# Kernel tuning notes

Measured on AMD Instinct MI355X. Metric: run time of the kernel, lower is better.

The kernel has to match this reference:

```python
import jax, jax.numpy as jnp
import numpy as np

EPS = 1e-5
HID = 32
FUSED = 33 * 33 * 33  # 35937


def _subnet(x, gamma, beta, W1, b1, W2, b2, W3, b3):
    # BatchNorm1d in training mode: batch mean / biased variance
    mu = jnp.mean(x, axis=0)
    var = jnp.mean((x - mu) ** 2, axis=0)
    xn = (x - mu) / jnp.sqrt(var + EPS) * gamma + beta
    h = jax.nn.relu(xn @ W1 + b1)
    h = jax.nn.relu(h @ W2 + b2)
    return jax.nn.relu(h @ W3 + b3)


def _subnet_params(key, in_dim):
    ks = jax.random.split(key, 6)
    s_in = 1.0 / np.sqrt(in_dim)
    s_h = 1.0 / np.sqrt(HID)
    return dict(
        gamma=jnp.ones((in_dim,), jnp.float32),
        beta=jnp.zeros((in_dim,), jnp.float32),
        W1=jax.random.uniform(ks[0], (in_dim, HID), jnp.float32, -s_in, s_in),
        b1=jax.random.uniform(ks[1], (HID,), jnp.float32, -s_in, s_in),
        W2=jax.random.uniform(ks[2], (HID, HID), jnp.float32, -s_h, s_h),
        b2=jax.random.uniform(ks[3], (HID,), jnp.float32, -s_h, s_h),
        W3=jax.random.uniform(ks[4], (HID, HID), jnp.float32, -s_h, s_h),
        b3=jax.random.uniform(ks[5], (HID,), jnp.float32, -s_h, s_h),
    )


def setup_inputs() -> dict:
    key = jax.random.key(0)
    ks = jax.random.split(key, 10)
    B = 8192
    inp = {
        'US_x': jax.random.normal(ks[0], (B, 1024), jnp.float32),
        'CDFI_x': jax.random.normal(ks[1], (B, 1024), jnp.float32),
        'marker_x': jax.random.normal(ks[2], (B, 10), jnp.float32),
    }
    for pref, k, d in (('us', ks[3], 1024), ('cd', ks[4], 1024), ('mk', ks[5], 10)):
        for n, v in _subnet_params(k, d).items():
            inp[f'{pref}_{n}'] = v
    s1 = 1.0 / np.sqrt(FUSED)
    s2 = 1.0 / np.sqrt(33)
    inp['Wf1'] = jax.random.uniform(ks[6], (FUSED, 33), jnp.float32, -s1, s1)
    inp['bf1'] = jax.random.uniform(ks[7], (33,), jnp.float32, -s1, s1)
    inp['Wf2'] = jax.random.uniform(ks[8], (33, 5), jnp.float32, -s2, s2)
    inp['bf2'] = jax.random.uniform(ks[9], (5,), jnp.float32, -s2, s2)
    return inp


def reference(US_x, CDFI_x, marker_x,
              us_gamma, us_beta, us_W1, us_b1, us_W2, us_b2, us_W3, us_b3,
              cd_gamma, cd_beta, cd_W1, cd_b1, cd_W2, cd_b2, cd_W3, cd_b3,
              mk_gamma, mk_beta, mk_W1, mk_b1, mk_W2, mk_b2, mk_W3, mk_b3,
              Wf1, bf1, Wf2, bf2):
    B = US_x.shape[0]
    us_h = _subnet(US_x, us_gamma, us_beta, us_W1, us_b1, us_W2, us_b2, us_W3, us_b3)
    cd_h = _subnet(CDFI_x, cd_gamma, cd_beta, cd_W1, cd_b1, cd_W2, cd_b2, cd_W3, cd_b3)
    mk_h = _subnet(marker_x, mk_gamma, mk_beta, mk_W1, mk_b1, mk_W2, mk_b2, mk_W3, mk_b3)
    ones = jnp.ones((B, 1), jnp.float32)
    us1 = jnp.concatenate([ones, us_h], axis=1)   # [B,33]
    cd1 = jnp.concatenate([ones, cd_h], axis=1)   # [B,33]
    mk1 = jnp.concatenate([ones, mk_h], axis=1)   # [B,33]
    # fused[b,k,j,i] = mk1[b,k] * cd1[b,j] * us1[b,i]; flattened row-major
    fused = jnp.einsum('bk,bj,bi->bkji', mk1, cd1, us1).reshape(B, FUSED)
    h = jax.nn.relu(fused @ Wf1 + bf1)
    return jax.nn.sigmoid(h @ Wf2 + bf2)
```

## Files before the change

kernel.cpp:

```cpp
#include <hip/hip_runtime.h>
#include <hip/hip_bf16.h>
#include <math.h>

typedef __hip_bfloat16 bf16;
typedef __attribute__((ext_vector_type(4))) float f32x4;
typedef __attribute__((ext_vector_type(8))) short s16x8;

#define NB 8192
#define KP 1152
#define NP 1152
#define NKT 18
#define SBLK 256

struct SubP {
    const float* x; const float* gamma; const float* beta;
    const float* W1; const float* b1; const float* W2; const float* b2;
    const float* W3; const float* b3;
    float* sum; float* sumsq; float* a; float* b1p; float* hout;
    bf16* w1t;
    int F;
};
struct SubP3 { SubP s[3]; };

__global__ void __launch_bounds__(256) stats3_kernel(SubP3 P) {
    const SubP p = P.s[blockIdx.z];
    int t = threadIdx.x;
    int blk = blockIdx.x;
    int row0 = blk * 32;
    if (p.F == 1024) {
        f32x4 s = {0.f, 0.f, 0.f, 0.f}, s2 = {0.f, 0.f, 0.f, 0.f};
        const float* xp = p.x + (size_t)row0 * 1024 + t * 4;
        #pragma unroll 8
        for (int r = 0; r < 32; r++) {
            f32x4 v = *(const f32x4*)(xp + (size_t)r * 1024);
            s += v; s2 += v * v;
        }
        int f = t * 4;
        *(f32x4*)&p.sum[(size_t)blk * 2048 + f]   = s;
        *(f32x4*)&p.sumsq[(size_t)blk * 2048 + f] = s2;
    } else {
        __shared__ float ls[16], ls2[16];
        if (t < 16) { ls[t] = 0.f; ls2[t] = 0.f; }
        __syncthreads();
        int F = p.F;
        for (int idx = t; idx < 32 * F; idx += 256) {
            float v = p.x[(size_t)row0 * F + idx];
            int f = idx % 10;
            atomicAdd(&ls[f], v);
            atomicAdd(&ls2[f], v * v);
        }
        __syncthreads();
        if (t < F) {
            p.sum[(size_t)blk * 2048 + t]   = ls[t];
            p.sumsq[(size_t)blk * 2048 + t] = ls2[t];
        }
    }
}

__global__ void prep3_kernel(SubP3 P) {
    const SubP p = P.s[blockIdx.y];
    int f0 = blockIdx.x * 32;
    if (f0 >= p.F) return;
    int t = threadIdx.x;
    __shared__ float c_sh[32];
    __shared__ float ash[32];
    __shared__ float red[8][33];
    __shared__ float rs[8][33], rs2[8][33];
    int fc = p.F - f0; if (fc > 32) fc = 32;
    int fi = t & 31, g = t >> 5;
    {
        float s = 0.f, s2 = 0.f;
        if (fi < fc) {
            for (int blk = g; blk < SBLK; blk += 8) {
                s  += p.sum[(size_t)blk * 2048 + f0 + fi];
                s2 += p.sumsq[(size_t)blk * 2048 + f0 + fi];
            }
        }
        rs[g][fi] = s; rs2[g][fi] = s2;
    }
    __syncthreads();
    if (t < 32) {
        float c = 0.f, av = 0.f;
        if (t < fc) {
            float sm = 0.f, sq = 0.f;
            #pragma unroll
            for (int gg = 0; gg < 8; gg++) { sm += rs[gg][t]; sq += rs2[gg][t]; }
            int f = f0 + t;
            float mu  = sm * (1.f / 8192.f);
            float var = sq * (1.f / 8192.f) - mu * mu;
            av = p.gamma[f] * rsqrtf(var + 1e-5f);
            p.a[f] = av;
            c = p.beta[f] - mu * av;
        }
        c_sh[t] = c; ash[t] = av;
    }
    __syncthreads();
    int h = t & 31; g = t >> 5;
    float s = 0.f;
    for (int fi2 = g; fi2 < fc; fi2 += 8)
        s += c_sh[fi2] * p.W1[(size_t)(f0 + fi2) * 32 + h];
    red[g][h] = s;
    __syncthreads();
    if (t < 32) {
        float tot = 0.f;
        #pragma unroll
        for (int gg = 0; gg < 8; gg++) tot += red[gg][t];
        atomicAdd(&p.b1p[t], tot);
    }
    if (p.F == 1024) {
        for (int idx = t; idx < 1024; idx += 256) {
            int kk = idx >> 5, hh = idx & 31;
            p.w1t[(size_t)hh * 1024 + f0 + kk] =
                __float2bfloat16(ash[kk] * p.W1[(size_t)(f0 + kk) * 32 + hh]);
        }
    }
}

__global__ void __launch_bounds__(256) subnet3_kernel(SubP3 P) {
    const SubP p = P.s[blockIdx.y];
    const int F = p.F;
    __shared__ float smem[9760];
    float* Red = smem;
    float* H1  = smem + 3456;
    float* W23 = smem + 4608;
    float* H2  = smem;

    int t = threadIdx.x;
    int row0 = blockIdx.x * 32;
    int kg = t >> 6;
    int lane = t & 63;
    int hg = lane & 7, h0 = hg * 4;
    int rg = (lane >> 3) & 3;
    int ks = lane >> 5;

    if (F == 1024) {
        bf16* Xl = (bf16*)(smem + 5664);
        bf16* Wl = (bf16*)(smem + 7712);
        int xr = t >> 3, xc = (t & 7) * 16;
        int sw = xr & 7;
        int s0 = ((t & 7) * 2) ^ sw, s1 = ((t & 7) * 2 + 1) ^ sw;
        const float* xbase = p.x + (size_t)(row0 + xr) * 1024 + xc;
        const bf16*  wbase = p.w1t + (size_t)xr * 1024 + xc;
        f32x4 xp[4]; s16x8 wp0, wp1;
        #pragma unroll
        for (int i = 0; i < 4; i++) xp[i] = *(const f32x4*)(xbase + i * 4);
        wp0 = *(const s16x8*)(wbase);
        wp1 = *(const s16x8*)(wbase + 8);

        f32x4 acc[2][2] = {};
        int fr = lane & 15, qq = lane >> 4;
        int rsw0 = fr & 7;

        for (int c = 0; c < 8; c++) {
            __builtin_amdgcn_s_barrier();
            asm volatile("" ::: "memory");
            {
                s16x8 v0, v1;
                #pragma unroll
                for (int i = 0; i < 2; i++)
                    #pragma unroll
                    for (int e = 0; e < 4; e++) {
                        __hip_bfloat16 hb = __float2bfloat16(xp[i][e]);
                        v0[i * 4 + e] = *(short*)&hb;
                    }
                #pragma unroll
                for (int i = 0; i < 2; i++)
                    #pragma unroll
                    for (int e = 0; e < 4; e++) {
                        __hip_bfloat16 hb = __float2bfloat16(xp[2 + i][e]);
                        v1[i * 4 + e] = *(short*)&hb;
                    }
                *(s16x8*)((char*)Xl + xr * 256 + s0 * 16) = v0;
                *(s16x8*)((char*)Xl + xr * 256 + s1 * 16) = v1;
                *(s16x8*)((char*)Wl + xr * 256 + s0 * 16) = wp0;
                *(s16x8*)((char*)Wl + xr * 256 + s1 * 16) = wp1;
            }
            if (c < 7) {
                int k0 = (c + 1) * 128;
                #pragma unroll
                for (int i = 0; i < 4; i++) xp[i] = *(const f32x4*)(xbase + k0 + i * 4);
                wp0 = *(const s16x8*)(wbase + k0);
                wp1 = *(const s16x8*)(wbase + k0 + 8);
            }
            asm volatile("s_waitcnt lgkmcnt(0)" ::: "memory");
            __builtin_amdgcn_sched_barrier(0);
            __builtin_amdgcn_s_barrier();
            asm volatile("" ::: "memory");
            {
                int sx = kg * 4 + qq;
                int sl = (sx ^ rsw0) * 16;
                s16x8 a0 = *(const s16x8*)((char*)Xl + fr * 256 + sl);
                s16x8 a1 = *(const s16x8*)((char*)Xl + (16 + fr) * 256 + sl);
                s16x8 b0 = *(const s16x8*)((char*)Wl + fr * 256 + sl);
                s16x8 b1 = *(const s16x8*)((char*)Wl + (16 + fr) * 256 + sl);
                acc[0][0] = __builtin_amdgcn_mfma_f32_16x16x32_bf16(a0, b0, acc[0][0], 0, 0, 0);
                acc[0][1] = __builtin_amdgcn_mfma_f32_16x16x32_bf16(a0, b1, acc[0][1], 0, 0, 0);
                acc[1][0] = __builtin_amdgcn_mfma_f32_16x16x32_bf16(a1, b0, acc[1][0], 0, 0, 0);
                acc[1][1] = __builtin_amdgcn_mfma_f32_16x16x32_bf16(a1, b1, acc[1][1], 0, 0, 0);
            }
        }
        int col = lane & 15, rowg = (lane >> 4) * 4;
        if (kg > 0) {
            #pragma unroll
            for (int m = 0; m < 2; m++)
                #pragma unroll
                for (int n = 0; n < 2; n++)
                    #pragma unroll
                    for (int r = 0; r < 4; r++)
                        Red[(kg - 1) * 1152 + (m * 16 + rowg + r) * 36 + n * 16 + col] = acc[m][n][r];
        }
        __syncthreads();
        if (kg == 0) {
            #pragma unroll
            for (int m = 0; m < 2; m++)
                #pragma unroll
                for (int n = 0; n < 2; n++) {
                    int cc = n * 16 + col;
                    float bv = p.b1[cc] + p.b1p[cc];
                    #pragma unroll
                    for (int r = 0; r < 4; r++) {
                        int rr = m * 16 + rowg + r;
                        float v = acc[m][n][r] + bv;
                        #pragma unroll
                        for (int pp = 0; pp < 3; pp++)
                            v += Red[pp * 1152 + rr * 36 + cc];
                        H1[rr * 36 + cc] = fmaxf(v, 0.f);
                    }
                }
        }
    } else {
        float* Xt = smem;
        float* Wt = smem + 2176;
        float acc[4][8] = {};
        int kbase = (kg * 2 + ks) * 8;
        for (int k0 = 0; k0 < F; k0 += 64) {
            int kc = F - k0; if (kc > 64) kc = 64;
            int kcp = (kc + 3) & ~3;
            __syncthreads();
            for (int idx = t; idx < 32 * kcp; idx += 256) {
                int r = idx / kcp, kk = idx - r * kcp;
                Xt[r * 68 + kk] = (kk < kc) ? p.x[(size_t)(row0 + r) * F + k0 + kk] : 0.f;
            }
            for (int idx = t; idx < kcp * 32; idx += 256) {
                int kk = idx >> 5, hh = idx & 31;
                Wt[kk * 36 + hh] = (kk < kc) ? p.a[k0 + kk] * p.W1[(size_t)(k0 + kk) * 32 + hh] : 0.f;
            }
            __syncthreads();
            #pragma unroll
            for (int s = 0; s < 2; s++) {
                int kk = kbase + s * 4;
                if (kk < kcp) {
                    f32x4 wv[4], xv[8];
                    #pragma unroll
                    for (int j = 0; j < 4; j++)  wv[j]  = *(const f32x4*)&Wt[(kk + j) * 36 + h0];
                    #pragma unroll
                    for (int ri = 0; ri < 8; ri++) xv[ri] = *(const f32x4*)&Xt[(rg + 4 * ri) * 68 + kk];
                    #pragma unroll
                    for (int j = 0; j < 4; j++)
                        #pragma unroll
                        for (int hi = 0; hi < 4; hi++) {
                            float w = wv[j][hi];
                            #pragma unroll
                            for (int ri = 0; ri < 8; ri++)
                                acc[hi][ri] = fmaf(w, xv[ri][j], acc[hi][ri]);
                        }
                }
            }
        }
        #pragma unroll
        for (int hi = 0; hi < 4; hi++)
            #pragma unroll
            for (int ri = 0; ri < 8; ri++)
                acc[hi][ri] += __shfl_xor(acc[hi][ri], 32);
        __syncthreads();
        if (kg > 0 && ks == 0) {
            #pragma unroll
            for (int ri = 0; ri < 8; ri++) {
                int r = rg + 4 * ri;
                f32x4 v = {acc[0][ri], acc[1][ri], acc[2][ri], acc[3][ri]};
                *(f32x4*)&Red[(kg - 1) * 1152 + r * 36 + h0] = v;
            }
        }
        __syncthreads();
        if (kg == 0 && ks == 0) {
            f32x4 b;
            #pragma unroll
            for (int hi = 0; hi < 4; hi++) b[hi] = p.b1[h0 + hi] + p.b1p[h0 + hi];
            #pragma unroll
            for (int ri = 0; ri < 8; ri++) {
                int r = rg + 4 * ri;
                f32x4 v = {acc[0][ri], acc[1][ri], acc[2][ri], acc[3][ri]};
                #pragma unroll
                for (int pp = 0; pp < 3; pp++)
                    v += *(const f32x4*)&Red[pp * 1152 + r * 36 + h0];
                v += b;
                #pragma unroll
                for (int hi = 0; hi < 4; hi++)
                    H1[r * 36 + h0 + hi] = fmaxf(v[hi], 0.f);
            }
        }
    }
    for (int idx = t; idx < 1024; idx += 256) W23[(idx >> 5) * 33 + (idx & 31)] = p.W2[idx];
    __syncthreads();
    int h = t & 31, rq = t >> 5;
    {
        float a2[4] = {};
        for (int q = 0; q < 32; q++) {
            float w = W23[q * 33 + h];
            #pragma unroll
            for (int i = 0; i < 4; i++) a2[i] += H1[(rq * 4 + i) * 36 + q] * w;
        }
        float bv = p.b2[h];
        #pragma unroll
        for (int i = 0; i < 4; i++) H2[(rq * 4 + i) * 36 + h] = fmaxf(a2[i] + bv, 0.f);
    }
    __syncthreads();
    for (int idx = t; idx < 1024; idx += 256) W23[(idx >> 5) * 33 + (idx & 31)] = p.W3[idx];
    __syncthreads();
    {
        float a3[4] = {};
        for (int q = 0; q < 32; q++) {
            float w = W23[q * 33 + h];
            #pragma unroll
            for (int i = 0; i < 4; i++) a3[i] += H2[(rq * 4 + i) * 36 + q] * w;
        }
        float bv = p.b3[h];
        #pragma unroll
        for (int i = 0; i < 4; i++)
            p.hout[(size_t)(row0 + rq * 4 + i) * 32 + h] = fmaxf(a3[i] + bv, 0.f);
    }
}

__global__ void __launch_bounds__(256) build_both(const float* __restrict__ mk_h,
                           const float* __restrict__ us_h,
                           bf16* __restrict__ p1,
                           const float* __restrict__ Wf1, bf16* __restrict__ W2t) {
    int blk = blockIdx.x;
    int t = threadIdx.x;
    if (blk < NB / 4) {
        int r = t >> 6, lane = t & 63;
        int b = blk * 4 + r;
        __shared__ float mk1[4][34], us1[4][34];
        if (lane == 0) { mk1[r][0] = 1.f; us1[r][0] = 1.f; }
        if (lane < 32) mk1[r][lane + 1] = mk_h[(size_t)b * 32 + lane];
        else           us1[r][lane - 31] = us_h[(size_t)b * 32 + (lane - 32)];
        __syncthreads();
        #pragma unroll
        for (int c = 0; c < 3; c++) {
            int chunk = lane + 64 * c;
            if (chunk < 144) {
                int base = chunk * 8;
                s16x8 v;
                #pragma unroll
                for (int e = 0; e < 8; e++) {
                    int idx = base + e;
                    float val = 0.f;
                    if (idx < 1089) {
                        int k = idx / 33, i = idx - k * 33;
                        val = mk1[r][k] * us1[r][i];
                    }
                    __hip_bfloat16 hb = __float2bfloat16(val);
                    v[e] = *(short*)&hb;
                }
                *(s16x8*)(p1 + (size_t)b * KP + base) = v;
            }
        }
    } else {
        int kj = blk - NB / 4;
        int k = kj / 33, j = kj - k * 33;
        __shared__ float tile[1089];
        const float* src = Wf1 + (size_t)k * 35937 + (size_t)j * 1089;
        for (int idx = t; idx < 1089; idx += 256) tile[idx] = src[idx];
        __syncthreads();
        for (int idx = t; idx < 1089; idx += 256) {
            int o = idx / 33, i = idx - o * 33;
            W2t[(size_t)(j * 33 + o) * KP + k * 33 + i] = __float2bfloat16(tile[i * 33 + o]);
        }
        if (k == 0) {
            bf16 z = __float2bfloat16(0.f);
            for (int idx = t; idx < 33 * 63; idx += 256) {
                int o = idx / 63, kkp = 1089 + idx - o * 63;
                W2t[(size_t)(j * 33 + o) * KP + kkp] = z;
            }
        }
    }
}

__global__ void __launch_bounds__(512) gemm_kernel(const bf16* __restrict__ A,
                                                   const bf16* __restrict__ Bt,
                                                   bf16* __restrict__ S) {
    __shared__ __align__(16) bf16 As[2][256 * 64];
    __shared__ __align__(16) bf16 Bs[2][192 * 64];
    int t = threadIdx.x;
    int wv = t >> 6, lane = t & 63;
    int m0 = blockIdx.x * 256;
    int n0 = blockIdx.y * 144;
    int fr = lane & 15;
    int q  = lane >> 4;
    int lr8 = lane >> 3;
    int sslot = (lane & 7) ^ lr8;

    const bf16* Ag = A  + (size_t)(m0 + wv * 32 + lr8) * KP + sslot * 8;
    const bf16* Bg = Bt + (size_t)(n0 + wv * 24 + lr8) * KP + sslot * 8;

    f32x4 acc[2][9] = {};

    auto stageA = [&](int buf, int T) {
        bf16* Ad = &As[buf][wv * 32 * 64];
        const bf16* s = Ag + T * 64;
        #pragma unroll
        for (int i = 0; i < 4; i++)
            __builtin_amdgcn_global_load_lds(
                (const __attribute__((address_space(1))) void*)(s + (size_t)i * 8 * KP),
                (__attribute__((address_space(3))) void*)(Ad + i * 512), 16, 0, 0);
    };
    auto stageB = [&](int buf, int T) {
        bf16* Bd = &Bs[buf][wv * 24 * 64];
        const bf16* s = Bg + T * 64;
        #pragma unroll
        for (int c = 0; c < 3; c++)
            __builtin_amdgcn_global_load_lds(
                (const __attribute__((address_space(1))) void*)(s + (size_t)c * 8 * KP),
                (__attribute__((address_space(3))) void*)(Bd + c * 512), 16, 0, 0);
    };

    stageA(0, 0);
    stageB(0, 0);

    for (int T = 0; T < NKT; T++) {
        int b = T & 1;
        const bf16* Ab = &As[b][0];
        const bf16* Bb = &Bs[b][0];
        if (T < NKT - 1) {
            stageA(b ^ 1, T + 1);
            asm volatile("s_waitcnt vmcnt(4)" ::: "memory");
        } else {
            asm volatile("s_waitcnt vmcnt(0)" ::: "memory");
        }
        __builtin_amdgcn_s_barrier();
        asm volatile("" ::: "memory");
        {
            int sl = (q ^ (fr & 7)) * 8;
            s16x8 af0 = *(const s16x8*)(Ab + (wv * 32 + fr) * 64 + sl);
            s16x8 af1 = *(const s16x8*)(Ab + (wv * 32 + 16 + fr) * 64 + sl);
            s16x8 bfv[9];
            #pragma unroll
            for (int n2 = 0; n2 < 9; n2++)
                bfv[n2] = *(const s16x8*)(Bb + (n2 * 16 + fr) * 64 + sl);
            __builtin_amdgcn_s_setprio(1);
            #pragma unroll
            for (int n2 = 0; n2 < 9; n2++) {
                acc[0][n2] = __builtin_amdgcn_mfma_f32_16x16x32_bf16(af0, bfv[n2], acc[0][n2], 0, 0, 0);
                acc[1][n2] = __builtin_amdgcn_mfma_f32_16x16x32_bf16(af1, bfv[n2], acc[1][n2], 0, 0, 0);
            }
            __builtin_amdgcn_s_setprio(0);
        }
        if (T < NKT - 1) stageB(b ^ 1, T + 1);
        {
            int sl = ((4 + q) ^ (fr & 7)) * 8;
            s16x8 af0 = *(const s16x8*)(Ab + (wv * 32 + fr) * 64 + sl);
            s16x8 af1 = *(const s16x8*)(Ab + (wv * 32 + 16 + fr) * 64 + sl);
            s16x8 bfv[9];
            #pragma unroll
            for (int n2 = 0; n2 < 9; n2++)
                bfv[n2] = *(const s16x8*)(Bb + (n2 * 16 + fr) * 64 + sl);
            __builtin_amdgcn_s_setprio(1);
            #pragma unroll
            for (int n2 = 0; n2 < 9; n2++) {
                acc[0][n2] = __builtin_amdgcn_mfma_f32_16x16x32_bf16(af0, bfv[n2], acc[0][n2], 0, 0, 0);
                acc[1][n2] = __builtin_amdgcn_mfma_f32_16x16x32_bf16(af1, bfv[n2], acc[1][n2], 0, 0, 0);
            }
            __builtin_amdgcn_s_setprio(0);
        }
        asm volatile("s_waitcnt lgkmcnt(0)" ::: "memory");
        __builtin_amdgcn_sched_barrier(0);
        __builtin_amdgcn_s_barrier();
        asm volatile("" ::: "memory");
    }

    int col = lane & 15, rowg = (lane >> 4) * 4;
    #pragma unroll
    for (int mt = 0; mt < 2; mt++)
        #pragma unroll
        for (int n2 = 0; n2 < 9; n2++)
            #pragma unroll
            for (int r = 0; r < 4; r++) {
                int gr = m0 + wv * 32 + mt * 16 + rowg + r;
                int gc = n0 + n2 * 16 + col;
                S[(size_t)gr * NP + gc] = __float2bfloat16(acc[mt][n2][r]);
            }
}

__global__ void __launch_bounds__(256) epilogue_kernel(const bf16* __restrict__ S,
                                const float* __restrict__ cd_h,
                                const float* __restrict__ bf1, const float* __restrict__ Wf2,
                                const float* __restrict__ bf2, float* __restrict__ out) {
    int w = threadIdx.x >> 6;
    int lane = threadIdx.x & 63;
    int b = blockIdx.x * 4 + w;
    __shared__ __align__(16) unsigned short Sl[4][1152];
    __shared__ float cdsh[4][33];
    __shared__ float hsh[4][40];
    const bf16* Srow = S + (size_t)b * NP;
    #pragma unroll
    for (int pass = 0; pass < 3; pass++) {
        int idx = lane + pass * 64;
        if (idx < 144)
            *(s16x8*)&Sl[w][idx * 8] = *(const s16x8*)(Srow + idx * 8);
    }
    if (lane == 0) cdsh[w][0] = 1.f;
    if (lane < 32) cdsh[w][lane + 1] = cd_h[(size_t)b * 32 + lane];
    __syncthreads();
    if (lane < 33) {
        float acc = bf1[lane];
        #pragma unroll 3
        for (int j = 0; j < 33; j++) {
            unsigned short sv = Sl[w][j * 33 + lane];
            acc += cdsh[w][j] * __bfloat162float(*(bf16*)&sv);
        }
        hsh[w][lane] = fmaxf(acc, 0.f);
    }
    __syncthreads();
    if (lane < 5) {
        float o = bf2[lane];
        for (int q = 0; q < 33; q++) o += hsh[w][q] * Wf2[q * 5 + lane];
        out[(size_t)b * 5 + lane] = 1.f / (1.f + expf(-o));
    }
}

extern "C" void kernel_launch(void* const* d_in, const int* in_sizes, int n_in,
                              void* d_out, int out_size, void* d_ws, size_t ws_size,
                              hipStream_t stream) {
    const float* US_x     = (const float*)d_in[0];
    const float* CDFI_x   = (const float*)d_in[1];
    const float* marker_x = (const float*)d_in[2];
    const float* Wf1      = (const float*)d_in[27];
    const float* bf1      = (const float*)d_in[28];
    const float* Wf2      = (const float*)d_in[29];
    const float* bf2      = (const float*)d_in[30];
    float* out = (float*)d_out;

    char* ws = (char*)d_ws;
    size_t off = 0;
    auto alloc = [&](size_t bytes) -> void* {
        void* p = ws + off;
        off = (off + bytes + 255) & ~(size_t)255;
        return p;
    };

    float* b1p_buf  = (float*)alloc(3 * 128 * sizeof(float));
    float* pstat    = (float*)alloc((size_t)3 * SBLK * 2048 * sizeof(float));
    bf16*  w1t_buf  = (bf16*)alloc((size_t)3 * 32 * 1024 * 2);
    float* a_buf[3], *h_buf[3];
    for (int i = 0; i < 3; i++) {
        a_buf[i] = (float*)alloc(1024 * 4);
        h_buf[i] = (float*)alloc((size_t)NB * 32 * 4);
    }
    bf16*  p1   = (bf16*)alloc((size_t)NB * KP * 2);
    bf16*  W2t  = (bf16*)alloc((size_t)NP * KP * 2);
    bf16*  S    = (bf16*)alloc((size_t)NB * NP * 2);

    SubP3 P;
    const float* xs[3] = {US_x, CDFI_x, marker_x};
    int Fs[3] = {1024, 1024, 10};
    for (int i = 0; i < 3; i++) {
        int base = 3 + i * 8;
        P.s[i].x     = xs[i];
        P.s[i].gamma = (const float*)d_in[base + 0];
        P.s[i].beta  = (const float*)d_in[base + 1];
        P.s[i].W1    = (const float*)d_in[base + 2];
        P.s[i].b1    = (const float*)d_in[base + 3];
        P.s[i].W2    = (const float*)d_in[base + 4];
        P.s[i].b2    = (const float*)d_in[base + 5];
        P.s[i].W3    = (const float*)d_in[base + 6];
        P.s[i].b3    = (const float*)d_in[base + 7];
        P.s[i].sum   = pstat + (size_t)i * SBLK * 2048;
        P.s[i].sumsq = pstat + (size_t)i * SBLK * 2048 + 1024;
        P.s[i].b1p   = b1p_buf + i * 128;
        P.s[i].a     = a_buf[i];
        P.s[i].hout  = h_buf[i];
        P.s[i].w1t   = w1t_buf + (size_t)i * 32 * 1024;
        P.s[i].F     = Fs[i];
    }

    float* us_h = h_buf[0];
    float* cd_h = h_buf[1];
    float* mk_h = h_buf[2];

    hipMemsetAsync(b1p_buf, 0, 3 * 128 * sizeof(float), stream);

    stats3_kernel<<<dim3(SBLK, 1, 3), 256, 0, stream>>>(P);
    prep3_kernel<<<dim3(32, 3), 256, 0, stream>>>(P);
    subnet3_kernel<<<dim3(256, 3), 256, 0, stream>>>(P);

    build_both<<<NB / 4 + 1089, 256, 0, stream>>>(mk_h, us_h, p1, Wf1, W2t);

    gemm_kernel<<<dim3(NB / 256, NP / 144), 512, 0, stream>>>(p1, W2t, S);

    epilogue_kernel<<<NB / 4, 256, 0, stream>>>(S, cd_h, bf1, Wf2, bf2, out);
}
```

Measured before the change: 235.5 us.

## Fuse cd_h contraction into GEMM epilogue, write per-block partial hidden sums

The GEMM no longer writes the full bf16 S matrix (8192x1152). Each block now contracts its accumulator tile with cd_h through LDS float atomics into per-row 33-wide partial sums and writes them as hpart. A small reduce kernel then sums the 8 column-block partials and applies bias, ReLU and the final layer. This removes a large intermediate write and its re-read, at the cost of LDS atomics and extra shared-memory reuse in the GEMM tail.

```diff
diff --git a/kernel.cpp b/kernel.cpp
--- a/kernel.cpp
+++ b/kernel.cpp
@@ -388,9 +388,11 @@
 
 __global__ void __launch_bounds__(512) gemm_kernel(const bf16* __restrict__ A,
                                                    const bf16* __restrict__ Bt,
-                                                   bf16* __restrict__ S) {
-    __shared__ __align__(16) bf16 As[2][256 * 64];
-    __shared__ __align__(16) bf16 Bs[2][192 * 64];
+                                                   const float* __restrict__ cd_h,
+                                                   float* __restrict__ hpart) {
+    __shared__ __align__(16) char ldsraw[114688];
+    bf16* As0 = (bf16*)ldsraw;
+    bf16* Bs0 = (bf16*)(ldsraw + 65536);
     int t = threadIdx.x;
     int wv = t >> 6, lane = t & 63;
     int m0 = blockIdx.x * 256;
@@ -406,7 +408,7 @@
     f32x4 acc[2][9] = {};
 
     auto stageA = [&](int buf, int T) {
-        bf16* Ad = &As[buf][wv * 32 * 64];
+        bf16* Ad = As0 + buf * 16384 + wv * 32 * 64;
         const bf16* s = Ag + T * 64;
         #pragma unroll
         for (int i = 0; i < 4; i++)
@@ -415,7 +417,7 @@
                 (__attribute__((address_space(3))) void*)(Ad + i * 512), 16, 0, 0);
     };
     auto stageB = [&](int buf, int T) {
-        bf16* Bd = &Bs[buf][wv * 24 * 64];
+        bf16* Bd = Bs0 + buf * 12288 + wv * 24 * 64;
         const bf16* s = Bg + T * 64;
         #pragma unroll
         for (int c = 0; c < 3; c++)
@@ -429,8 +431,8 @@
 
     for (int T = 0; T < NKT; T++) {
         int b = T & 1;
-        const bf16* Ab = &As[b][0];
-        const bf16* Bb = &Bs[b][0];
+        const bf16* Ab = As0 + b * 16384;
+        const bf16* Bb = Bs0 + b * 12288;
         if (T < NKT - 1) {
             stageA(b ^ 1, T + 1);
             asm volatile("s_waitcnt vmcnt(4)" ::: "memory");
@@ -478,47 +480,52 @@
         asm volatile("" ::: "memory");
     }
 
-    int col = lane & 15, rowg = (lane >> 4) * 4;
-    #pragma unroll
-    for (int mt = 0; mt < 2; mt++)
-        #pragma unroll
-        for (int n2 = 0; n2 < 9; n2++)
-            #pragma unroll
-            for (int r = 0; r < 4; r++) {
-                int gr = m0 + wv * 32 + mt * 16 + rowg + r;
-                int gc = n0 + n2 * 16 + col;
-                S[(size_t)gr * NP + gc] = __float2bfloat16(acc[mt][n2][r]);
-            }
+    float* hacc = (float*)ldsraw;
+    float* cdl  = (float*)(ldsraw + 33792);
+    for (int idx = t; idx < 8448; idx += 512) hacc[idx] = 0.f;
+    for (int idx = t; idx < 8448; idx += 512) {
+        int row = idx / 33, j = idx - row * 33;
+        cdl[idx] = (j == 0) ? 1.f : cd_h[(size_t)(m0 + row) * 32 + (j - 1)];
+    }
+    __syncthreads();
+    {
+        int col = lane & 15, rowg4 = (lane >> 4) * 4;
+        #pragma unroll
+        for (int n2 = 0; n2 < 9; n2++) {
+            int gc = n0 + n2 * 16 + col;
+            if (gc < 1089) {
+                int j = gc / 33;
+                int o = gc - j * 33;
+                #pragma unroll
+                for (int mt = 0; mt < 2; mt++)
+                    #pragma unroll
+                    for (int r = 0; r < 4; r++) {
+                        int lrow = wv * 32 + mt * 16 + rowg4 + r;
+                        atomicAdd(&hacc[lrow * 33 + o], cdl[lrow * 33 + j] * acc[mt][n2][r]);
+                    }
+            }
+        }
+    }
+    __syncthreads();
+    for (int idx = t; idx < 8448; idx += 512) {
+        int row = idx / 33, o = idx - row * 33;
+        hpart[(size_t)(m0 + row) * 264 + blockIdx.y * 33 + o] = hacc[idx];
+    }
 }
 
-__global__ void __launch_bounds__(256) epilogue_kernel(const bf16* __restrict__ S,
-                                const float* __restrict__ cd_h,
+__global__ void __launch_bounds__(256) reduce_out(const float* __restrict__ hpart,
                                 const float* __restrict__ bf1, const float* __restrict__ Wf2,
                                 const float* __restrict__ bf2, float* __restrict__ out) {
     int w = threadIdx.x >> 6;
     int lane = threadIdx.x & 63;
     int b = blockIdx.x * 4 + w;
-    __shared__ __align__(16) unsigned short Sl[4][1152];
-    __shared__ float cdsh[4][33];
     __shared__ float hsh[4][40];
-    const bf16* Srow = S + (size_t)b * NP;
-    #pragma unroll
-    for (int pass = 0; pass < 3; pass++) {
-        int idx = lane + pass * 64;
-        if (idx < 144)
-            *(s16x8*)&Sl[w][idx * 8] = *(const s16x8*)(Srow + idx * 8);
-    }
-    if (lane == 0) cdsh[w][0] = 1.f;
-    if (lane < 32) cdsh[w][lane + 1] = cd_h[(size_t)b * 32 + lane];
-    __syncthreads();
     if (lane < 33) {
-        float acc = bf1[lane];
-        #pragma unroll 3
-        for (int j = 0; j < 33; j++) {
-            unsigned short sv = Sl[w][j * 33 + lane];
-            acc += cdsh[w][j] * __bfloat162float(*(bf16*)&sv);
-        }
-        hsh[w][lane] = fmaxf(acc, 0.f);
+        const float* hp = hpart + (size_t)b * 264 + lane;
+        float a = bf1[lane];
+        #pragma unroll
+        for (int nb = 0; nb < 8; nb++) a += hp[nb * 33];
+        hsh[w][lane] = fmaxf(a, 0.f);
     }
     __syncthreads();
     if (lane < 5) {
@@ -558,7 +565,7 @@
     }
     bf16*  p1   = (bf16*)alloc((size_t)NB * KP * 2);
     bf16*  W2t  = (bf16*)alloc((size_t)NP * KP * 2);
-    bf16*  S    = (bf16*)alloc((size_t)NB * NP * 2);
+    float* hpart = (float*)alloc((size_t)NB * 264 * 4);
 
     SubP3 P;
     const float* xs[3] = {US_x, CDFI_x, marker_x};
@@ -595,7 +602,7 @@
 
     build_both<<<NB / 4 + 1089, 256, 0, stream>>>(mk_h, us_h, p1, Wf1, W2t);
 
-    gemm_kernel<<<dim3(NB / 256, NP / 144), 512, 0, stream>>>(p1, W2t, S);
-
-    epilogue_kernel<<<NB / 4, 256, 0, stream>>>(S, cd_h, bf1, Wf2, bf2, out);
+    gemm_kernel<<<dim3(NB / 256, NP / 144), 512, 0, stream>>>(p1, W2t, cd_h, hpart);
+
+    reduce_out<<<NB / 4, 256, 0, stream>>>(hpart, bf1, Wf2, bf2, out);
 }
```

New measurement: 267.7 us. 1.14x slower.
